# Kernel tuning notes

Hardware: AMD Instinct MI355X
Metric: run time of the kernel (lower is better)

The kernel has to match this reference:

```python
import jax, jax.numpy as jnp
import numpy as np

EPS = 1e-5

def _ln(x, g, b):
    mu = jnp.mean(x, axis=-1, keepdims=True)
    var = jnp.mean(jnp.square(x - mu), axis=-1, keepdims=True)
    return (x - mu) * jax.lax.rsqrt(var + EPS) * g + b

def setup_inputs() -> dict:
    BS, LN, FS = 64, 256, 512
    H, OUT, ATT, L = 1024, 128, 256, 8
    key = jax.random.key(0)
    ks = jax.random.split(key, 8)
    s = 0.02
    inp = {
        "x": jax.random.normal(ks[0], (BS, LN, FS), jnp.float32),
        # fc stem
        "ln0_g": jnp.ones((FS,), jnp.float32),
        "ln0_b": jnp.zeros((FS,), jnp.float32),
        "W0": jax.random.normal(ks[1], (FS, H), jnp.float32) * s,
        "b0": jnp.zeros((H,), jnp.float32),
        # residual blocks (stacked)
        "res_ln_g": jnp.ones((L, H), jnp.float32),
        "res_ln_b": jnp.zeros((L, H), jnp.float32),
        "res_W": jax.random.normal(ks[2], (L, H, H), jnp.float32) * s,
        "res_b": jnp.zeros((L, H), jnp.float32),
        # fc head
        "lnf_g": jnp.ones((H,), jnp.float32),
        "lnf_b": jnp.zeros((H,), jnp.float32),
        "Wf": jax.random.normal(ks[3], (H, OUT), jnp.float32) * s,
        "bf": jnp.zeros((OUT,), jnp.float32),
        # attention MLP over time axis
        "a_ln1_g": jnp.ones((LN + 1,), jnp.float32),
        "a_ln1_b": jnp.zeros((LN + 1,), jnp.float32),
        "Wa1": jax.random.normal(ks[4], (LN + 1, ATT), jnp.float32) * s,
        "ba1": jnp.zeros((ATT,), jnp.float32),
        "a_ln2_g": jnp.ones((ATT,), jnp.float32),
        "a_ln2_b": jnp.zeros((ATT,), jnp.float32),
        "Wa2": jax.random.normal(ks[5], (ATT, LN), jnp.float32) * s,
        "ba2": jnp.zeros((LN,), jnp.float32),
    }
    return inp

def reference(x, ln0_g, ln0_b, W0, b0, res_ln_g, res_ln_b, res_W, res_b,
              lnf_g, lnf_b, Wf, bf, a_ln1_g, a_ln1_b, Wa1, ba1,
              a_ln2_g, a_ln2_b, Wa2, ba2):
    # fc trunk (dropout is identity in eval)
    h = jax.nn.relu(_ln(x, ln0_g, ln0_b) @ W0 + b0)          # [bs, ln, H]
    for i in range(res_W.shape[0]):
        h = h + jax.nn.relu(_ln(h, res_ln_g[i], res_ln_b[i]) @ res_W[i] + res_b[i])
    fc_out = _ln(h, lnf_g, lnf_b) @ Wf + bf                  # [bs, ln, out]

    # attention: batched over (bs, out) instead of python loop
    mean = jnp.mean(fc_out, axis=1, keepdims=True)           # [bs, 1, out]
    t = jnp.concatenate([fc_out, mean], axis=1).transpose(0, 2, 1)  # [bs, out, ln+1]
    a = jax.nn.relu(_ln(t, a_ln1_g, a_ln1_b) @ Wa1 + ba1)    # [bs, out, att]
    w = _ln(a, a_ln2_g, a_ln2_b) @ Wa2 + ba2                 # [bs, out, ln]
    w = jax.nn.softmax(w, axis=2).transpose(0, 2, 1)         # [bs, ln, out]

    # einsum('ijk,ijk->ik')
    return jnp.sum(fc_out * w, axis=1)                        # [bs, out]
```

## Files before the change

kernel.cpp:

```cpp
#include <hip/hip_runtime.h>
#include <hip/hip_bf16.h>
#include <stdint.h>

#define EPSV 1e-5f

typedef int i32x4 __attribute__((ext_vector_type(4)));

__device__ __forceinline__ void gload_lds16(const void* g, void* l) {
    __builtin_amdgcn_global_load_lds(
        (const __attribute__((address_space(1))) uint32_t*)g,
        (__attribute__((address_space(3))) uint32_t*)l, 16, 0, 0);
}

__device__ __forceinline__ float block_sum256(float v, float* red) {
#pragma unroll
    for (int off = 32; off; off >>= 1) v += __shfl_down(v, off);
    int lane = threadIdx.x & 63, w = threadIdx.x >> 6;
    __syncthreads();
    if (lane == 0) red[w] = v;
    __syncthreads();
    return red[0] + red[1] + red[2] + red[3];
}

__global__ __launch_bounds__(256)
void ln_quant(const float* __restrict__ X, const float* __restrict__ g,
              const float* __restrict__ b, uint8_t* __restrict__ Aq,
              float* __restrict__ sA, int D) {
    __shared__ float red[4];
    __shared__ float ybuf[1024];
    int row = blockIdx.x;
    const float* x = X + (size_t)row * D;
    int tid = threadIdx.x;
    int nvec = D >> 2;

    float s = 0.f, sq = 0.f;
    for (int i = tid; i < nvec; i += 256) {
        float4 v = ((const float4*)x)[i];
        s += v.x + v.y + v.z + v.w;
        sq += v.x * v.x + v.y * v.y + v.z * v.z + v.w * v.w;
    }
    float ts = block_sum256(s, red);
    float tq = block_sum256(sq, red);
    float invD = 1.f / (float)D;
    float mu = ts * invD;
    float rstd = rsqrtf(tq * invD - mu * mu + EPSV);

    float mx = 0.f;
    for (int i = tid; i < nvec; i += 256) {
        float4 v = ((const float4*)x)[i];
        float4 gv = ((const float4*)g)[i];
        float4 bv = ((const float4*)b)[i];
        float4 y;
        y.x = (v.x - mu) * rstd * gv.x + bv.x;
        y.y = (v.y - mu) * rstd * gv.y + bv.y;
        y.z = (v.z - mu) * rstd * gv.z + bv.z;
        y.w = (v.w - mu) * rstd * gv.w + bv.w;
        *(float4*)&ybuf[4 * i] = y;
        mx = fmaxf(mx, fmaxf(fmaxf(fabsf(y.x), fabsf(y.y)),
                             fmaxf(fabsf(y.z), fabsf(y.w))));
    }
#pragma unroll
    for (int off = 32; off; off >>= 1) mx = fmaxf(mx, __shfl_down(mx, off));
    int lane = tid & 63, w = tid >> 6;
    __syncthreads();
    if (lane == 0) red[w] = mx;
    __syncthreads();
    float rmax = fmaxf(fmaxf(fmaxf(red[0], red[1]), fmaxf(red[2], red[3])), 1e-30f);
    float inv = 127.f / rmax;
    if (tid == 0) sA[row] = rmax * (1.f / 127.f);

    uint8_t* arow = Aq + (size_t)row * ((size_t)D * 2);
    for (int i = tid; i < nvec; i += 256) {
        float4 y = *(float4*)&ybuf[4 * i];
        float qv[4] = { y.x * inv, y.y * inv, y.z * inv, y.w * inv };
        uint32_t u1 = 0, u2 = 0;
#pragma unroll
        for (int j = 0; j < 4; ++j) {
            float q1 = rintf(qv[j]);
            float q2 = rintf((qv[j] - q1) * 128.f);
            u1 |= ((uint32_t)((int)q1 & 0xFF)) << (8 * j);
            u2 |= ((uint32_t)((int)q2 & 0xFF)) << (8 * j);
        }
        int kt = i >> 4;
        int o = (i & 15) * 4;
        *(uint32_t*)(arow + kt * 128 + o) = u1;
        *(uint32_t*)(arow + kt * 128 + 64 + o) = u2;
    }
}

__global__ __launch_bounds__(256)
void col_absmax(const float* __restrict__ W, float* __restrict__ part,
                int K, int N) {
    int n = blockIdx.y * 256 + threadIdx.x;
    int kp = blockIdx.x;
    if (n >= N) return;
    int kc = K >> 3;
    int k0 = kp * kc;
    float m = 0.f;
    for (int k = k0; k < k0 + kc; ++k)
        m = fmaxf(m, fabsf(W[(size_t)k * N + n]));
    part[kp * N + n] = m;
}

__global__ __launch_bounds__(256)
void col_scale(const float* __restrict__ part, float* __restrict__ sB, int N) {
    int n = blockIdx.x * 256 + threadIdx.x;
    if (n >= N) return;
    float m = 0.f;
#pragma unroll
    for (int kp = 0; kp < 8; ++kp) m = fmaxf(m, part[kp * N + n]);
    m = fmaxf(m, 1e-30f);
    sB[n] = m * (1.f / 127.f);
}

__global__ __launch_bounds__(64)
void conv_wq(const float* __restrict__ W, const float* __restrict__ sB,
             uint8_t* __restrict__ Wq, int K, int N) {
    int n = blockIdx.x * 64 + threadIdx.x;
    int kt = blockIdx.y;
    if (n >= N) return;
    float inv = 1.f / sB[n];
    uint32_t u1[16], u2[16];
#pragma unroll 4
    for (int o = 0; o < 16; ++o) {
        uint32_t a = 0, bq = 0;
#pragma unroll
        for (int j = 0; j < 4; ++j) {
            float q = W[(size_t)(kt * 64 + o * 4 + j) * N + n] * inv;
            float q1 = rintf(q);
            float q2 = rintf((q - q1) * 128.f);
            a |= ((uint32_t)((int)q1 & 0xFF)) << (8 * j);
            bq |= ((uint32_t)((int)q2 & 0xFF)) << (8 * j);
        }
        u1[o] = a; u2[o] = bq;
    }
    uint8_t* wrow = Wq + (size_t)n * ((size_t)K * 2) + kt * 128;
    uint4* d = (uint4*)wrow;
    const uint4* p1 = (const uint4*)u1;
    const uint4* p2 = (const uint4*)u2;
    d[0] = p1[0]; d[1] = p1[1]; d[2] = p1[2]; d[3] = p1[3];
    d[4] = p2[0]; d[5] = p2[1]; d[6] = p2[2]; d[7] = p2[3];
}

__global__ __launch_bounds__(256)
void col_absmax_rw(const float* __restrict__ rW, float* __restrict__ part) {
    int c = blockIdx.y * 256 + threadIdx.x;
    int kp = blockIdx.x;
    int layer = c >> 10, n = c & 1023;
    const float* W = rW + ((size_t)layer << 20);
    int k0 = kp * 128;
    float m = 0.f;
    for (int k = k0; k < k0 + 128; ++k)
        m = fmaxf(m, fabsf(W[(size_t)k * 1024 + n]));
    part[kp * 8192 + c] = m;
}

__global__ __launch_bounds__(256)
void col_scale_rw(const float* __restrict__ part, float* __restrict__ sB) {
    int c = blockIdx.x * 256 + threadIdx.x;
    float m = 0.f;
#pragma unroll
    for (int kp = 0; kp < 8; ++kp) m = fmaxf(m, part[kp * 8192 + c]);
    m = fmaxf(m, 1e-30f);
    sB[c] = m * (1.f / 127.f);
}

__global__ __launch_bounds__(64)
void conv_wq_rw(const float* __restrict__ rW, const float* __restrict__ sB,
                uint8_t* __restrict__ Wq) {
    int c = blockIdx.x * 64 + threadIdx.x;
    int kt = blockIdx.y;
    int layer = c >> 10, n = c & 1023;
    const float* W = rW + ((size_t)layer << 20);
    float inv = 1.f / sB[c];
    uint32_t u1[16], u2[16];
#pragma unroll 4
    for (int o = 0; o < 16; ++o) {
        uint32_t a = 0, bq = 0;
#pragma unroll
        for (int j = 0; j < 4; ++j) {
            float q = W[(size_t)(kt * 64 + o * 4 + j) * 1024 + n] * inv;
            float q1 = rintf(q);
            float q2 = rintf((q - q1) * 128.f);
            a |= ((uint32_t)((int)q1 & 0xFF)) << (8 * j);
            bq |= ((uint32_t)((int)q2 & 0xFF)) << (8 * j);
        }
        u1[o] = a; u2[o] = bq;
    }
    uint8_t* wrow = Wq + ((size_t)layer << 21) + (size_t)n * 2048 + kt * 128;
    uint4* d = (uint4*)wrow;
    const uint4* p1 = (const uint4*)u1;
    const uint4* p2 = (const uint4*)u2;
    d[0] = p1[0]; d[1] = p1[1]; d[2] = p1[2]; d[3] = p1[3];
    d[4] = p2[0]; d[5] = p2[1]; d[6] = p2[2]; d[7] = p2[3];
}

template <int MODE, bool KSPLIT = false>
__global__ __launch_bounds__(512, 2)
void gemm_i8(const uint8_t* __restrict__ Aq, const uint8_t* __restrict__ Bq,
             const float* __restrict__ sA, const float* __restrict__ sB,
             const float* __restrict__ bias, float* __restrict__ C,
             int M, int N, int K) {
    __shared__ char Abuf[2][32768];
    __shared__ char Bbuf[2][16384];

    const int tid = threadIdx.x;
    const int lane = tid & 63;
    const int wv = tid >> 6;
    const int wr = wv >> 1;
    const int wc = wv & 1;

    int m0, n0, nt;
    size_t kbyte0;
    float* Cout;
    if constexpr (KSPLIT) {
        m0 = blockIdx.x * 256;
        n0 = 0;
        int half = K >> 1;
        nt = half >> 6;
        kbyte0 = (size_t)blockIdx.y * half * 2;
        Cout = C + (size_t)blockIdx.y * M * N;
    } else {
        int lid = blockIdx.y * gridDim.x + blockIdx.x;
        int nwg = gridDim.x * gridDim.y;
        int chunk = nwg >> 3;
        int swz = (lid & 7) * chunk + (lid >> 3);
        int nIdx = swz % gridDim.y;
        int mIdx = swz / gridDim.y;
        m0 = mIdx * 256; n0 = nIdx * 128;
        nt = K >> 6;
        kbyte0 = 0;
        Cout = C;
    }

    const size_t rowB = (size_t)K * 2;

    int arow[4], aq[4];
#pragma unroll
    for (int i = 0; i < 4; ++i) {
        int s = i * 512 + tid;
        arow[i] = s >> 3;
        aq[i] = (s & 7) ^ (arow[i] & 7);
    }
    int brow[2], bq[2];
#pragma unroll
    for (int i = 0; i < 2; ++i) {
        int s = i * 512 + tid;
        brow[i] = s >> 3;
        bq[i] = (s & 7) ^ (brow[i] & 7);
    }

    i32x4 accP[4][4] = {};
    i32x4 accQ[4][4] = {};

#pragma unroll
    for (int i = 0; i < 4; ++i)
        gload_lds16((const char*)Aq + (size_t)(m0 + arow[i]) * rowB + kbyte0 + aq[i] * 16,
                    Abuf[0] + (i * 512 + tid) * 16);
#pragma unroll
    for (int i = 0; i < 2; ++i)
        gload_lds16((const char*)Bq + (size_t)(n0 + brow[i]) * rowB + kbyte0 + bq[i] * 16,
                    Bbuf[0] + (i * 512 + tid) * 16);
    __syncthreads();

    int p = 0;
    const int g = lane >> 4;
    const int rr = lane & 15;

    for (int kt = 0; kt < nt; ++kt) {
        if (kt + 1 < nt) {
            const size_t koff = kbyte0 + (size_t)(kt + 1) * 128;
#pragma unroll
            for (int i = 0; i < 4; ++i)
                gload_lds16((const char*)Aq + (size_t)(m0 + arow[i]) * rowB + koff + aq[i] * 16,
                            Abuf[p ^ 1] + (i * 512 + tid) * 16);
#pragma unroll
            for (int i = 0; i < 2; ++i)
                gload_lds16((const char*)Bq + (size_t)(n0 + brow[i]) * rowB + koff + bq[i] * 16,
                            Bbuf[p ^ 1] + (i * 512 + tid) * 16);
        }

        const char* Ab = Abuf[p];
        const char* Bb = Bbuf[p];

        i32x4 a1[4], b1[4];
#pragma unroll
        for (int m = 0; m < 4; ++m) {
            int rA = wr * 64 + m * 16 + rr;
            a1[m] = *(const i32x4*)(Ab + rA * 128 + ((g ^ (rA & 7)) * 16));
        }
#pragma unroll
        for (int n = 0; n < 4; ++n) {
            int rB = wc * 64 + n * 16 + rr;
            b1[n] = *(const i32x4*)(Bb + rB * 128 + ((g ^ (rB & 7)) * 16));
        }
#pragma unroll
        for (int m = 0; m < 4; ++m)
#pragma unroll
            for (int n = 0; n < 4; ++n)
                accP[m][n] = __builtin_amdgcn_mfma_i32_16x16x64_i8(a1[m], b1[n], accP[m][n], 0, 0, 0);

        {
            i32x4 b2[4];
#pragma unroll
            for (int n = 0; n < 4; ++n) {
                int rB = wc * 64 + n * 16 + rr;
                b2[n] = *(const i32x4*)(Bb + rB * 128 + (((g + 4) ^ (rB & 7)) * 16));
            }
#pragma unroll
            for (int m = 0; m < 4; ++m)
#pragma unroll
                for (int n = 0; n < 4; ++n)
                    accQ[m][n] = __builtin_amdgcn_mfma_i32_16x16x64_i8(a1[m], b2[n], accQ[m][n], 0, 0, 0);
        }
        {
            i32x4 a2[4];
#pragma unroll
            for (int m = 0; m < 4; ++m) {
                int rA = wr * 64 + m * 16 + rr;
                a2[m] = *(const i32x4*)(Ab + rA * 128 + (((g + 4) ^ (rA & 7)) * 16));
            }
#pragma unroll
            for (int m = 0; m < 4; ++m)
#pragma unroll
                for (int n = 0; n < 4; ++n)
                    accQ[m][n] = __builtin_amdgcn_mfma_i32_16x16x64_i8(a2[m], b1[n], accQ[m][n], 0, 0, 0);
        }

        __syncthreads();
        p ^= 1;
    }

#pragma unroll
    for (int m = 0; m < 4; ++m) {
        int rbase = m0 + wr * 64 + m * 16 + (lane >> 4) * 4;
#pragma unroll
        for (int n = 0; n < 4; ++n) {
            int c = n0 + wc * 64 + n * 16 + (lane & 15);
            float sbc = sB[c];
            float bv = bias[c];
            if (KSPLIT && blockIdx.y != 0) bv = 0.f;
#pragma unroll
            for (int j = 0; j < 4; ++j) {
                int r = rbase + j;
                float v = sA[r] * sbc *
                          ((float)accP[m][n][j] + 0.0078125f * (float)accQ[m][n][j]) + bv;
                float* cp = &Cout[(size_t)r * N + c];
                if (MODE == 0) *cp = fmaxf(v, 0.f);
                else if (MODE == 1) *cp = *cp + fmaxf(v, 0.f);
                else *cp = v;
            }
        }
    }
}

template <bool MAXOP>
__device__ __forceinline__ void red8(const float* v, float* out, float (*scr)[4]) {
    int lane = threadIdx.x & 63, wv = threadIdx.x >> 6, tid = threadIdx.x;
#pragma unroll
    for (int oo = 0; oo < 8; ++oo) {
        float r = v[oo];
#pragma unroll
        for (int m = 1; m < 64; m <<= 1) {
            float t = __shfl_xor(r, m);
            r = MAXOP ? fmaxf(r, t) : r + t;
        }
        if (lane == 0) scr[oo][wv] = r;
    }
    __syncthreads();
    if (tid < 8) {
        float a = scr[tid][0], b = scr[tid][1], c = scr[tid][2], d = scr[tid][3];
        out[tid] = MAXOP ? fmaxf(fmaxf(a, b), fmaxf(c, d)) : (a + b + c + d);
    }
    __syncthreads();
}

__global__ __launch_bounds__(256)
void attn_g8(const float* __restrict__ fc01,
             const float* __restrict__ g1, const float* __restrict__ b1,
             const float* __restrict__ Wa1, const float* __restrict__ ba1,
             const float* __restrict__ g2, const float* __restrict__ b2,
             const float* __restrict__ Wa2, const float* __restrict__ ba2,
             float* __restrict__ out) {
    __shared__ float buf[257][12];
    __shared__ float scr[8][4];
    __shared__ float sS[8], sQ[8], sO[8];

    const int R128 = 16384 * 128;
    int bs = blockIdx.x >> 4;
    int o0 = (blockIdx.x & 15) * 8;
    int tid = threadIdx.x;
    int jgrp = tid >> 1;
    int kp = tid & 1;

    float vv[8], tmp[8];
    size_t base = (size_t)(bs * 256 + tid) * 128 + o0;
    const float4* fp0 = (const float4*)(fc01 + base);
    const float4* fp1 = (const float4*)(fc01 + R128 + base);
#pragma unroll
    for (int q = 0; q < 2; ++q) {
        float4 t0 = fp0[q];
        float4 t1 = fp1[q];
        vv[4 * q] = t0.x + t1.x; vv[4 * q + 1] = t0.y + t1.y;
        vv[4 * q + 2] = t0.z + t1.z; vv[4 * q + 3] = t0.w + t1.w;
    }

#pragma unroll
    for (int oo = 0; oo < 8; ++oo) tmp[oo] = vv[oo] * vv[oo];
    red8<false>(vv, sS, scr);
    red8<false>(tmp, sQ, scr);

    float gl = g1[tid], bl = b1[tid];
#pragma unroll
    for (int oo = 0; oo < 8; ++oo) {
        float s = sS[oo], q = sQ[oo];
        float mean = s * (1.f / 256.f);
        float mu = (s + mean) * (1.f / 257.f);
        float var = (q + mean * mean) * (1.f / 257.f) - mu * mu;
        float rstd = rsqrtf(var + EPSV);
        tmp[oo] = (vv[oo] - mu) * rstd * gl + bl;
    }
#pragma unroll
    for (int q = 0; q < 2; ++q)
        *(float4*)&buf[tid][4 * q] = *(float4*)&tmp[4 * q];
    if (tid < 8) {
        int oo = tid;
        float s = sS[oo], q = sQ[oo];
        float mean = s * (1.f / 256.f);
        float mu = (s + mean) * (1.f / 257.f);
        float var = (q + mean * mean) * (1.f / 257.f) - mu * mu;
        float rstd = rsqrtf(var + EPSV);
        buf[256][oo] = (mean - mu) * rstd * g1[256] + b1[256];
    }
    __syncthreads();

    float acc1[8][2] = {};
#pragma unroll 2
    for (int i = 0; i < 128; ++i) {
        int k = 2 * i + kp;
        float2 wv2 = *(const float2*)&Wa1[(size_t)k * 256 + jgrp * 2];
        float4 t0 = *(const float4*)&buf[k][0];
        float4 t1 = *(const float4*)&buf[k][4];
        float bv[8] = { t0.x, t0.y, t0.z, t0.w, t1.x, t1.y, t1.z, t1.w };
#pragma unroll
        for (int oo = 0; oo < 8; ++oo) {
            acc1[oo][0] = fmaf(bv[oo], wv2.x, acc1[oo][0]);
            acc1[oo][1] = fmaf(bv[oo], wv2.y, acc1[oo][1]);
        }
    }
    if (kp == 0) {
        float2 wv2 = *(const float2*)&Wa1[(size_t)256 * 256 + jgrp * 2];
#pragma unroll
        for (int oo = 0; oo < 8; ++oo) {
            float bv = buf[256][oo];
            acc1[oo][0] = fmaf(bv, wv2.x, acc1[oo][0]);
            acc1[oo][1] = fmaf(bv, wv2.y, acc1[oo][1]);
        }
    }
    float a_[8];
#pragma unroll
    for (int oo = 0; oo < 8; ++oo) {
        float p0 = acc1[oo][0] + __shfl_xor(acc1[oo][0], 1);
        float p1 = acc1[oo][1] + __shfl_xor(acc1[oo][1], 1);
        a_[oo] = kp ? p1 : p0;
    }
    float bb = ba1[tid];
#pragma unroll
    for (int oo = 0; oo < 8; ++oo) a_[oo] = fmaxf(a_[oo] + bb, 0.f);

#pragma unroll
    for (int oo = 0; oo < 8; ++oo) tmp[oo] = a_[oo] * a_[oo];
    red8<false>(a_, sS, scr);
    red8<false>(tmp, sQ, scr);

    float g2l = g2[tid], b2l = b2[tid];
#pragma unroll
    for (int oo = 0; oo < 8; ++oo) {
        float mu2 = sS[oo] * (1.f / 256.f);
        float rstd2 = rsqrtf(sQ[oo] * (1.f / 256.f) - mu2 * mu2 + EPSV);
        tmp[oo] = (a_[oo] - mu2) * rstd2 * g2l + b2l;
    }
#pragma unroll
    for (int q = 0; q < 2; ++q)
        *(float4*)&buf[tid][4 * q] = *(float4*)&tmp[4 * q];
    __syncthreads();

    float acc2[8][2] = {};
#pragma unroll 2
    for (int i = 0; i < 128; ++i) {
        int k = 2 * i + kp;
        float2 wv2 = *(const float2*)&Wa2[(size_t)k * 256 + jgrp * 2];
        float4 t0 = *(const float4*)&buf[k][0];
        float4 t1 = *(const float4*)&buf[k][4];
        float bv[8] = { t0.x, t0.y, t0.z, t0.w, t1.x, t1.y, t1.z, t1.w };
#pragma unroll
        for (int oo = 0; oo < 8; ++oo) {
            acc2[oo][0] = fmaf(bv[oo], wv2.x, acc2[oo][0]);
            acc2[oo][1] = fmaf(bv[oo], wv2.y, acc2[oo][1]);
        }
    }
    float w_[8];
#pragma unroll
    for (int oo = 0; oo < 8; ++oo) {
        float p0 = acc2[oo][0] + __shfl_xor(acc2[oo][0], 1);
        float p1 = acc2[oo][1] + __shfl_xor(acc2[oo][1], 1);
        w_[oo] = kp ? p1 : p0;
    }
    float bb2 = ba2[tid];
#pragma unroll
    for (int oo = 0; oo < 8; ++oo) w_[oo] += bb2;

    red8<true>(w_, sO, scr);
    float e_[8];
#pragma unroll
    for (int oo = 0; oo < 8; ++oo) e_[oo] = __expf(w_[oo] - sO[oo]);
    red8<false>(e_, sS, scr);
#pragma unroll
    for (int oo = 0; oo < 8; ++oo) tmp[oo] = vv[oo] * e_[oo] / sS[oo];
    red8<false>(tmp, sQ, scr);
    if (tid < 8) out[bs * 128 + o0 + tid] = sQ[tid];
}

extern "C" void kernel_launch(void* const* d_in, const int* in_sizes, int n_in,
                              void* d_out, int out_size, void* d_ws, size_t ws_size,
                              hipStream_t stream) {
    const float* x      = (const float*)d_in[0];
    const float* ln0_g  = (const float*)d_in[1];
    const float* ln0_b  = (const float*)d_in[2];
    const float* W0     = (const float*)d_in[3];
    const float* b0     = (const float*)d_in[4];
    const float* rln_g  = (const float*)d_in[5];
    const float* rln_b  = (const float*)d_in[6];
    const float* rW     = (const float*)d_in[7];
    const float* rb     = (const float*)d_in[8];
    const float* lnf_g  = (const float*)d_in[9];
    const float* lnf_b  = (const float*)d_in[10];
    const float* Wf     = (const float*)d_in[11];
    const float* bf_    = (const float*)d_in[12];
    const float* ln1_g  = (const float*)d_in[13];
    const float* ln1_b  = (const float*)d_in[14];
    const float* Wa1    = (const float*)d_in[15];
    const float* ba1    = (const float*)d_in[16];
    const float* ln2_g  = (const float*)d_in[17];
    const float* ln2_b  = (const float*)d_in[18];
    const float* Wa2    = (const float*)d_in[19];
    const float* ba2    = (const float*)d_in[20];
    float* out = (float*)d_out;

    const int R = 64 * 256;
    float*    h     = (float*)d_ws;
    uint8_t*  Aq    = (uint8_t*)(h + (size_t)R * 1024);
    float*    fc01  = (float*)(Aq + (size_t)R * 2048);
    uint8_t*  Wq0   = (uint8_t*)(fc01 + (size_t)2 * R * 128);
    uint8_t*  WqR   = Wq0 + (size_t)1024 * 1024;
    uint8_t*  Wqf   = WqR + (size_t)8 * 1024 * 2048;
    float*    sA    = (float*)(Wqf + (size_t)128 * 2048);
    float*    sB0   = sA + R;
    float*    sBR   = sB0 + 1024;
    float*    sBf   = sBR + 8192;
    float*    part  = sBf + 128;

    col_absmax<<<dim3(8, 4), 256, 0, stream>>>(W0, part, 512, 1024);
    col_scale<<<4, 256, 0, stream>>>(part, sB0, 1024);
    conv_wq<<<dim3(16, 8), 64, 0, stream>>>(W0, sB0, Wq0, 512, 1024);

    col_absmax_rw<<<dim3(8, 32), 256, 0, stream>>>(rW, part);
    col_scale_rw<<<32, 256, 0, stream>>>(part, sBR);
    conv_wq_rw<<<dim3(128, 16), 64, 0, stream>>>(rW, sBR, WqR);

    col_absmax<<<dim3(8, 1), 256, 0, stream>>>(Wf, part, 1024, 128);
    col_scale<<<1, 256, 0, stream>>>(part, sBf, 128);
    conv_wq<<<dim3(2, 16), 64, 0, stream>>>(Wf, sBf, Wqf, 1024, 128);

    ln_quant<<<R, 256, 0, stream>>>(x, ln0_g, ln0_b, Aq, sA, 512);
    gemm_i8<0><<<dim3(64, 8), 512, 0, stream>>>(Aq, Wq0, sA, sB0, b0, h, R, 1024, 512);

    for (int i = 0; i < 8; ++i) {
        ln_quant<<<R, 256, 0, stream>>>(h, rln_g + i * 1024, rln_b + i * 1024, Aq, sA, 1024);
        gemm_i8<1><<<dim3(64, 8), 512, 0, stream>>>(
            Aq, WqR + ((size_t)i << 21), sA, sBR + i * 1024, rb + i * 1024, h, R, 1024, 1024);
    }

    ln_quant<<<R, 256, 0, stream>>>(h, lnf_g, lnf_b, Aq, sA, 1024);
    gemm_i8<2, true><<<dim3(64, 2), 512, 0, stream>>>(Aq, Wqf, sA, sBf, bf_, fc01, R, 128, 1024);

    attn_g8<<<64 * 16, 256, 0, stream>>>(fc01, ln1_g, ln1_b, Wa1, ba1,
                                         ln2_g, ln2_b, Wa2, ba2, out);
}
```

Measured before the change: 1.102 ms.

## Single-buffer int8 GEMM LDS and widen attention k-split to four lanes

The int8 GEMM drops its double-buffered LDS prefetch and becomes a single-buffered loop: each k-tile is loaded, then synchronised, then computed. This halves LDS use, which may allow more blocks to reside per CU, but global loads no longer overlap with MFMA work. Separately, the attention kernel splits the K dimension across four lanes instead of two, so each thread reads float4 weights and computes four output columns. This needs extra shuffle reductions and more accumulator registers.

Result: slower. 1.254 ms (+13.8%).

```diff
diff --git a/kernel.cpp b/kernel.cpp
--- a/kernel.cpp
+++ b/kernel.cpp
@@ -201,8 +201,8 @@
              const float* __restrict__ sA, const float* __restrict__ sB,
              const float* __restrict__ bias, float* __restrict__ C,
              int M, int N, int K) {
-    __shared__ char Abuf[2][32768];
-    __shared__ char Bbuf[2][16384];
+    __shared__ char Abuf[32768];
+    __shared__ char Bbuf[16384];
 
     const int tid = threadIdx.x;
     const int lane = tid & 63;
@@ -253,46 +253,32 @@
     i32x4 accP[4][4] = {};
     i32x4 accQ[4][4] = {};
 
-#pragma unroll
-    for (int i = 0; i < 4; ++i)
-        gload_lds16((const char*)Aq + (size_t)(m0 + arow[i]) * rowB + kbyte0 + aq[i] * 16,
-                    Abuf[0] + (i * 512 + tid) * 16);
-#pragma unroll
-    for (int i = 0; i < 2; ++i)
-        gload_lds16((const char*)Bq + (size_t)(n0 + brow[i]) * rowB + kbyte0 + bq[i] * 16,
-                    Bbuf[0] + (i * 512 + tid) * 16);
-    __syncthreads();
-
-    int p = 0;
     const int g = lane >> 4;
     const int rr = lane & 15;
 
     for (int kt = 0; kt < nt; ++kt) {
-        if (kt + 1 < nt) {
-            const size_t koff = kbyte0 + (size_t)(kt + 1) * 128;
-#pragma unroll
-            for (int i = 0; i < 4; ++i)
-                gload_lds16((const char*)Aq + (size_t)(m0 + arow[i]) * rowB + koff + aq[i] * 16,
-                            Abuf[p ^ 1] + (i * 512 + tid) * 16);
-#pragma unroll
-            for (int i = 0; i < 2; ++i)
-                gload_lds16((const char*)Bq + (size_t)(n0 + brow[i]) * rowB + koff + bq[i] * 16,
-                            Bbuf[p ^ 1] + (i * 512 + tid) * 16);
-        }
-
-        const char* Ab = Abuf[p];
-        const char* Bb = Bbuf[p];
+        __syncthreads();
+        const size_t koff = kbyte0 + (size_t)kt * 128;
+#pragma unroll
+        for (int i = 0; i < 4; ++i)
+            gload_lds16((const char*)Aq + (size_t)(m0 + arow[i]) * rowB + koff + aq[i] * 16,
+                        Abuf + (i * 512 + tid) * 16);
+#pragma unroll
+        for (int i = 0; i < 2; ++i)
+            gload_lds16((const char*)Bq + (size_t)(n0 + brow[i]) * rowB + koff + bq[i] * 16,
+                        Bbuf + (i * 512 + tid) * 16);
+        __syncthreads();
 
         i32x4 a1[4], b1[4];
 #pragma unroll
         for (int m = 0; m < 4; ++m) {
             int rA = wr * 64 + m * 16 + rr;
-            a1[m] = *(const i32x4*)(Ab + rA * 128 + ((g ^ (rA & 7)) * 16));
+            a1[m] = *(const i32x4*)(Abuf + rA * 128 + ((g ^ (rA & 7)) * 16));
         }
 #pragma unroll
         for (int n = 0; n < 4; ++n) {
             int rB = wc * 64 + n * 16 + rr;
-            b1[n] = *(const i32x4*)(Bb + rB * 128 + ((g ^ (rB & 7)) * 16));
+            b1[n] = *(const i32x4*)(Bbuf + rB * 128 + ((g ^ (rB & 7)) * 16));
         }
 #pragma unroll
         for (int m = 0; m < 4; ++m)
@@ -305,7 +291,7 @@
 #pragma unroll
             for (int n = 0; n < 4; ++n) {
                 int rB = wc * 64 + n * 16 + rr;
-                b2[n] = *(const i32x4*)(Bb + rB * 128 + (((g + 4) ^ (rB & 7)) * 16));
+                b2[n] = *(const i32x4*)(Bbuf + rB * 128 + (((g + 4) ^ (rB & 7)) * 16));
             }
 #pragma unroll
             for (int m = 0; m < 4; ++m)
@@ -318,7 +304,7 @@
 #pragma unroll
             for (int m = 0; m < 4; ++m) {
                 int rA = wr * 64 + m * 16 + rr;
-                a2[m] = *(const i32x4*)(Ab + rA * 128 + (((g + 4) ^ (rA & 7)) * 16));
+                a2[m] = *(const i32x4*)(Abuf + rA * 128 + (((g + 4) ^ (rA & 7)) * 16));
             }
 #pragma unroll
             for (int m = 0; m < 4; ++m)
@@ -326,9 +312,6 @@
                 for (int n = 0; n < 4; ++n)
                     accQ[m][n] = __builtin_amdgcn_mfma_i32_16x16x64_i8(a2[m], b1[n], accQ[m][n], 0, 0, 0);
         }
-
-        __syncthreads();
-        p ^= 1;
     }
 
 #pragma unroll
@@ -390,8 +373,8 @@
     int bs = blockIdx.x >> 4;
     int o0 = (blockIdx.x & 15) * 8;
     int tid = threadIdx.x;
-    int jgrp = tid >> 1;
-    int kp = tid & 1;
+    int jgrp = tid >> 2;
+    int kp = tid & 3;
 
     float vv[8], tmp[8];
     size_t base = (size_t)(bs * 256 + tid) * 128 + o0;
@@ -434,35 +417,44 @@
     }
     __syncthreads();
 
-    float acc1[8][2] = {};
+    float acc1[8][4] = {};
 #pragma unroll 2
-    for (int i = 0; i < 128; ++i) {
-        int k = 2 * i + kp;
-        float2 wv2 = *(const float2*)&Wa1[(size_t)k * 256 + jgrp * 2];
+    for (int i = 0; i < 64; ++i) {
+        int k = 4 * i + kp;
+        float4 w4 = *(const float4*)&Wa1[(size_t)k * 256 + jgrp * 4];
         float4 t0 = *(const float4*)&buf[k][0];
         float4 t1 = *(const float4*)&buf[k][4];
         float bv[8] = { t0.x, t0.y, t0.z, t0.w, t1.x, t1.y, t1.z, t1.w };
 #pragma unroll
         for (int oo = 0; oo < 8; ++oo) {
-            acc1[oo][0] = fmaf(bv[oo], wv2.x, acc1[oo][0]);
-            acc1[oo][1] = fmaf(bv[oo], wv2.y, acc1[oo][1]);
+            acc1[oo][0] = fmaf(bv[oo], w4.x, acc1[oo][0]);
+            acc1[oo][1] = fmaf(bv[oo], w4.y, acc1[oo][1]);
+            acc1[oo][2] = fmaf(bv[oo], w4.z, acc1[oo][2]);
+            acc1[oo][3] = fmaf(bv[oo], w4.w, acc1[oo][3]);
         }
     }
     if (kp == 0) {
-        float2 wv2 = *(const float2*)&Wa1[(size_t)256 * 256 + jgrp * 2];
+        float4 w4 = *(const float4*)&Wa1[(size_t)256 * 256 + jgrp * 4];
 #pragma unroll
         for (int oo = 0; oo < 8; ++oo) {
             float bv = buf[256][oo];
-            acc1[oo][0] = fmaf(bv, wv2.x, acc1[oo][0]);
-            acc1[oo][1] = fmaf(bv, wv2.y, acc1[oo][1]);
+            acc1[oo][0] = fmaf(bv, w4.x, acc1[oo][0]);
+            acc1[oo][1] = fmaf(bv, w4.y, acc1[oo][1]);
+            acc1[oo][2] = fmaf(bv, w4.z, acc1[oo][2]);
+            acc1[oo][3] = fmaf(bv, w4.w, acc1[oo][3]);
         }
     }
     float a_[8];
 #pragma unroll
     for (int oo = 0; oo < 8; ++oo) {
-        float p0 = acc1[oo][0] + __shfl_xor(acc1[oo][0], 1);
-        float p1 = acc1[oo][1] + __shfl_xor(acc1[oo][1], 1);
-        a_[oo] = kp ? p1 : p0;
+#pragma unroll
+        for (int jj = 0; jj < 4; ++jj) {
+            acc1[oo][jj] += __shfl_xor(acc1[oo][jj], 1);
+            acc1[oo][jj] += __shfl_xor(acc1[oo][jj], 2);
+        }
+        float v01 = (kp & 1) ? acc1[oo][1] : acc1[oo][0];
+        float v23 = (kp & 1) ? acc1[oo][3] : acc1[oo][2];
+        a_[oo] = (kp & 2) ? v23 : v01;
     }
     float bb = ba1[tid];
 #pragma unroll
@@ -485,26 +477,33 @@
         *(float4*)&buf[tid][4 * q] = *(float4*)&tmp[4 * q];
     __syncthreads();
 
-    float acc2[8][2] = {};
+    float acc2[8][4] = {};
 #pragma unroll 2
-    for (int i = 0; i < 128; ++i) {
-        int k = 2 * i + kp;
-        float2 wv2 = *(const float2*)&Wa2[(size_t)k * 256 + jgrp * 2];
+    for (int i = 0; i < 64; ++i) {
+        int k = 4 * i + kp;
+        float4 w4 = *(const float4*)&Wa2[(size_t)k * 256 + jgrp * 4];
         float4 t0 = *(const float4*)&buf[k][0];
         float4 t1 = *(const float4*)&buf[k][4];
         float bv[8] = { t0.x, t0.y, t0.z, t0.w, t1.x, t1.y, t1.z, t1.w };
 #pragma unroll
         for (int oo = 0; oo < 8; ++oo) {
-            acc2[oo][0] = fmaf(bv[oo], wv2.x, acc2[oo][0]);
-            acc2[oo][1] = fmaf(bv[oo], wv2.y, acc2[oo][1]);
+            acc2[oo][0] = fmaf(bv[oo], w4.x, acc2[oo][0]);
+            acc2[oo][1] = fmaf(bv[oo], w4.y, acc2[oo][1]);
+            acc2[oo][2] = fmaf(bv[oo], w4.z, acc2[oo][2]);
+            acc2[oo][3] = fmaf(bv[oo], w4.w, acc2[oo][3]);
         }
     }
     float w_[8];
 #pragma unroll
     for (int oo = 0; oo < 8; ++oo) {
-        float p0 = acc2[oo][0] + __shfl_xor(acc2[oo][0], 1);
-        float p1 = acc2[oo][1] + __shfl_xor(acc2[oo][1], 1);
-        w_[oo] = kp ? p1 : p0;
+#pragma unroll
+        for (int jj = 0; jj < 4; ++jj) {
+            acc2[oo][jj] += __shfl_xor(acc2[oo][jj], 1);
+            acc2[oo][jj] += __shfl_xor(acc2[oo][jj], 2);
+        }
+        float v01 = (kp & 1) ? acc2[oo][1] : acc2[oo][0];
+        float v23 = (kp & 1) ? acc2[oo][3] : acc2[oo][2];
+        w_[oo] = (kp & 2) ? v23 : v01;
     }
     float bb2 = ba2[tid];
 #pragma unroll
```
